# Kernel optimization log

Hardware: AMD Instinct MI355X
Metric: run time of the kernel (lower is better)

Reference implementation:

```python
import jax, jax.numpy as jnp
import numpy as np

B, S, HID, NH = 2, 2048, 1024, 16
HD = HID // NH
SCALE = HD ** -0.5


def elu_plus_one(x):
    return jax.nn.elu(x) + 1.0


def setup_inputs() -> dict:
    key = jax.random.key(0)
    ks = jax.random.split(key, 8)
    w_scale = 0.02  # keep logits in a sane range
    return {
        "hidden_states": jax.random.normal(ks[0], (B, S, HID), jnp.float32),
        "wq": jax.random.normal(ks[1], (HID, HID), jnp.float32) * w_scale,
        "wk": jax.random.normal(ks[2], (HID, HID), jnp.float32) * w_scale,
        "wv": jax.random.normal(ks[3], (HID, HID), jnp.float32) * w_scale,
        "wo": jax.random.normal(ks[4], (HID, HID), jnp.float32) * w_scale,
        "beta": jax.random.normal(ks[5], (NH,), jnp.float32),
        "memory": jax.random.normal(ks[6], (NH, HD, HD), jnp.float32),
        "memory_norm": jax.random.uniform(ks[7], (NH, HD), jnp.float32),
    }


def reference(hidden_states, wq, wk, wv, wo, beta, memory, memory_norm):
    b, s, _ = hidden_states.shape
    # nn.Linear(bias=False): x @ W^T; weights stored [out, in]
    def proj(x, w):
        return jnp.einsum("bsh,oh->bso", x, w).reshape(b, s, NH, HD).transpose(0, 2, 1, 3)

    q = proj(hidden_states, wq)  # [B,H,S,D]
    k = proj(hidden_states, wk)
    v = proj(hidden_states, wv)

    # local causal softmax attention (materializes [B,H,S,S] as the original does)
    scores = jnp.einsum("bhsd,bhtd->bhst", q, k) * SCALE
    causal_mask = jnp.triu(jnp.full((s, s), -jnp.inf, dtype=scores.dtype), k=1)
    attn = jax.nn.softmax(scores + causal_mask, axis=-1)
    a_local = jnp.einsum("bhst,bhtd->bhsd", attn, v)

    # compressive memory retrieval: sigma(Q) @ M / (sigma(Q) @ z)
    sigma_q = elu_plus_one(q)
    a_mem_unnorm = jnp.einsum("bhsd,hde->bhse", sigma_q, memory)
    norm = jnp.clip(jnp.einsum("bhsd,hd->bhs", sigma_q, memory_norm), 1e-6, None)
    a_mem = a_mem_unnorm / norm[..., None]

    gate = jax.nn.sigmoid(beta).reshape(1, NH, 1, 1)
    combined = gate * a_mem + (1.0 - gate) * a_local  # [B,H,S,D]
    combined = combined.transpose(0, 2, 1, 3).reshape(b, s, HID)
    return jnp.einsum("bsh,oh->bso", combined, wo)
```

## Files before the change

kernel.cpp:

```cpp
#include <hip/hip_runtime.h>
#include <stdint.h>

#define LOG2E 1.4426950408889634f

typedef __attribute__((ext_vector_type(8))) __bf16 bf16x8;
typedef __attribute__((ext_vector_type(4))) __bf16 bf16x4;
typedef __attribute__((ext_vector_type(4))) float f32x4;

__device__ inline void gll16(const void* g, void* l) {
  __builtin_amdgcn_global_load_lds(
      (const __attribute__((address_space(1))) void*)g,
      (__attribute__((address_space(3))) void*)l, 16, 0, 0);
}

__global__ __launch_bounds__(256) void cvt_all(
    const float* __restrict__ hs, const float* __restrict__ wq,
    const float* __restrict__ wk, const float* __restrict__ wv,
    const float* __restrict__ wo,
    __bf16* __restrict__ hsb, __bf16* __restrict__ wqb, __bf16* __restrict__ wkb,
    __bf16* __restrict__ wvb, __bf16* __restrict__ wob) {
  int bid = blockIdx.x;
  const float* s; __bf16* d; int i;
  if (bid < 4096) { s = hs; d = hsb; i = bid * 256 + threadIdx.x; }
  else {
    int seg = (bid - 4096) >> 10;
    i = ((bid - 4096) & 1023) * 256 + threadIdx.x;
    s = seg == 0 ? wq : seg == 1 ? wk : seg == 2 ? wv : wo;
    d = seg == 0 ? wqb : seg == 1 ? wkb : seg == 2 ? wvb : wob;
  }
  float4 v = ((const float4*)s)[i];
  bf16x4 o;
  o[0] = (__bf16)v.x; o[1] = (__bf16)v.y; o[2] = (__bf16)v.z; o[3] = (__bf16)v.w;
  *(bf16x4*)&d[(size_t)i * 4] = o;
}

#define KSCALE 0.18033688011112042f
#define QSWZ(row, col) (((row) << 6) + ((col) ^ (((row) & 7) << 3)))

__global__ __launch_bounds__(256, 3) void qkv_gemm(
    const __bf16* __restrict__ hsb, const __bf16* __restrict__ wqb,
    const __bf16* __restrict__ wkb, const __bf16* __restrict__ wvb,
    __bf16* __restrict__ qbuf, __bf16* __restrict__ kbuf,
    __bf16* __restrict__ vtb) {
  constexpr int K = 1024;
  __shared__ __align__(16) __bf16 lta[128 * 64];
  __shared__ __align__(16) __bf16 ltb[128 * 64];
  const int bid = blockIdx.x;
  const int z = bid >> 8, r = bid & 255;
  const __bf16 *A, *Bt;
  int m0, n0;
  if (z < 2) {
    A = hsb; Bt = z ? wkb : wqb;
    m0 = (r & 31) * 128; n0 = (r >> 5) * 128;
  } else {
    A = wvb; Bt = hsb;
    m0 = (r & 7) * 128; n0 = (r >> 3) * 128;
  }
  const int tid = threadIdx.x;
  const int w = tid >> 6, l = tid & 63;
  const int lg = l >> 4, lr = l & 15;
  const int wm = (w >> 1) * 64, wn = (w & 1) * 64;
  f32x4 acc[4][4] = {};
  const int srow = tid >> 3;
  const int scol = ((tid & 7) ^ ((tid >> 3) & 7)) * 8;
  const __bf16* ga = A + (size_t)(m0 + srow) * K + scol;
  const __bf16* gb = Bt + (size_t)(n0 + srow) * K + scol;
  for (int k0 = 0; k0 < K; k0 += 64) {
    __syncthreads();
#pragma unroll
    for (int p = 0; p < 4; ++p) {
      gll16(ga + (size_t)p * 32 * K + k0, &lta[p * 2048 + w * 512]);
      gll16(gb + (size_t)p * 32 * K + k0, &ltb[p * 2048 + w * 512]);
    }
    __syncthreads();
#pragma unroll
    for (int kk = 0; kk < 2; ++kk) {
      bf16x8 af[4], bfr[4];
#pragma unroll
      for (int i = 0; i < 4; ++i) {
        af[i]  = *(const bf16x8*)&lta[QSWZ(wm + i * 16 + lr, kk * 32 + lg * 8)];
        bfr[i] = *(const bf16x8*)&ltb[QSWZ(wn + i * 16 + lr, kk * 32 + lg * 8)];
      }
#pragma unroll
      for (int i = 0; i < 4; ++i)
#pragma unroll
        for (int j = 0; j < 4; ++j)
          acc[i][j] = __builtin_amdgcn_mfma_f32_16x16x32_bf16(af[i], bfr[j], acc[i][j], 0, 0, 0);
    }
  }
#pragma unroll
  for (int i = 0; i < 4; ++i)
#pragma unroll
    for (int j = 0; j < 4; ++j)
#pragma unroll
      for (int rr = 0; rr < 4; ++rr) {
        int gm = m0 + wm + i * 16 + lg * 4 + rr;
        int gn = n0 + wn + j * 16 + lr;
        float v = acc[i][j][rr];
        if (z < 2) {
          int bb = gm >> 11, s = gm & 2047, hh = gn >> 6, d = gn & 63;
          __bf16* dst = z ? kbuf : qbuf;
          if (z) v *= KSCALE;
          dst[(((size_t)bb * 16 + hh) * 2048 + s) * 64 + d] = (__bf16)v;
        } else {
          int bb = gn >> 11, s = gn & 2047, hh = gm >> 6, d = gm & 63;
          vtb[(((size_t)bb * 16 + hh) * 64 + d) * 2048 + s] = (__bf16)v;
        }
      }
}

__global__ __launch_bounds__(256, 4) void gemm_out(const __bf16* __restrict__ A,
                                                   const __bf16* __restrict__ Bt,
                                                   float* __restrict__ C,
                                                   int M, int N) {
  constexpr int K = 1024;
  __shared__ __align__(16) __bf16 lta[128 * 64];
  __shared__ __align__(16) __bf16 ltb[64 * 64];
  const int tid = threadIdx.x;
  const int w = tid >> 6, l = tid & 63;
  const int lg = l >> 4, lr = l & 15;
  const int m0 = blockIdx.x * 128, n0 = blockIdx.y * 64;
  const int wm = (w >> 1) * 64, wn = (w & 1) * 32;
  f32x4 acc[4][2] = {};
  const int srow = tid >> 3;
  const int scol = ((tid & 7) ^ ((tid >> 3) & 7)) * 8;
  const __bf16* ga = A + (size_t)(m0 + srow) * K + scol;
  const __bf16* gb = Bt + (size_t)(n0 + srow) * K + scol;
  for (int k0 = 0; k0 < K; k0 += 64) {
    __syncthreads();
#pragma unroll
    for (int p = 0; p < 4; ++p)
      gll16(ga + (size_t)p * 32 * K + k0, &lta[p * 2048 + w * 512]);
#pragma unroll
    for (int p = 0; p < 2; ++p)
      gll16(gb + (size_t)p * 32 * K + k0, &ltb[p * 2048 + w * 512]);
    __syncthreads();
#pragma unroll
    for (int kk = 0; kk < 2; ++kk) {
      bf16x8 af[4], bfr[2];
#pragma unroll
      for (int i = 0; i < 4; ++i)
        af[i]  = *(const bf16x8*)&lta[QSWZ(wm + i * 16 + lr, kk * 32 + lg * 8)];
#pragma unroll
      for (int j = 0; j < 2; ++j)
        bfr[j] = *(const bf16x8*)&ltb[QSWZ(wn + j * 16 + lr, kk * 32 + lg * 8)];
#pragma unroll
      for (int i = 0; i < 4; ++i)
#pragma unroll
        for (int j = 0; j < 2; ++j)
          acc[i][j] = __builtin_amdgcn_mfma_f32_16x16x32_bf16(af[i], bfr[j], acc[i][j], 0, 0, 0);
    }
  }
#pragma unroll
  for (int i = 0; i < 4; ++i)
#pragma unroll
    for (int j = 0; j < 2; ++j)
#pragma unroll
      for (int rr = 0; rr < 4; ++rr) {
        int gm = m0 + wm + i * 16 + lg * 4 + rr;
        int gn = n0 + wn + j * 16 + lr;
        C[(size_t)gm * N + gn] = acc[i][j][rr];
      }
}

#define DEFER_THR 11.5f
#define SWZ(row, col) (((row) << 7) + ((col) ^ (((row) & 7) << 3)))
#define SWZK(row, col) (((row) << 6) + ((col) ^ (((row) & 7) << 3)))

__global__ __launch_bounds__(256, 5) void attn_kernel(
    const __bf16* __restrict__ qb,
    const __bf16* __restrict__ kb,
    const __bf16* __restrict__ vtb,
    const float* __restrict__ memory,
    const float* __restrict__ memnorm,
    const float* __restrict__ beta,
    __bf16* __restrict__ comb)
{
  __shared__ __align__(16) __bf16 kt[128 * 64];
  __shared__ __align__(16) __bf16 vt[64 * 128];

  const int tid = threadIdx.x;
  const int w = tid >> 6, l = tid & 63;
  const int lg = l >> 4, lr = l & 15;
  const int t = 31 - (blockIdx.x >> 5);
  const int bh = blockIdx.x & 31;
  const int hh = bh & 15, b = bh >> 4;
  const int wq0 = t * 64 + w * 16;
  const int ntiles = (t >> 1) + 1;

  const int k_row = tid >> 3;
  const int k_col = ((tid & 7) ^ (k_row & 7)) * 8;
  const __bf16* ksrc = kb + ((size_t)bh * 2048 + k_row) * 64 + k_col;
  const int v_d = tid >> 4;
  const int v_col = ((tid & 15) ^ (v_d & 7)) * 8;
  const __bf16* vsrc = vtb + ((size_t)bh * 64 + v_d) * 2048 + v_col;
  __bf16* kdst = &kt[w * 512];
  __bf16* vdst = &vt[w * 512];

  bf16x8 qf[2];
#pragma unroll
  for (int kk = 0; kk < 2; ++kk)
    qf[kk] = *(const bf16x8*)(qb + ((size_t)bh * 2048 + wq0 + lr) * 64 + kk * 32 + lg * 8);

  float mrun = -1e30f, lsum = 0.f;
  f32x4 apv[4] = {};

  for (int kv = 0; kv < ntiles; ++kv) {
    const int kv0 = kv * 128;
    __syncthreads();
#pragma unroll
    for (int i = 0; i < 4; ++i)
      gll16(ksrc + (size_t)(kv0 + i * 32) * 64, kdst + i * 2048);
#pragma unroll
    for (int i = 0; i < 4; ++i)
      gll16(vsrc + (size_t)i * 16 * 2048 + kv0, vdst + i * 2048);
    asm volatile("s_waitcnt vmcnt(4)" ::: "memory");
    __builtin_amdgcn_sched_barrier(0);
    __builtin_amdgcn_s_barrier();

    f32x4 sc[8] = {};
    __builtin_amdgcn_s_setprio(1);
#pragma unroll
    for (int kk = 0; kk < 2; ++kk)
#pragma unroll
      for (int nf = 0; nf < 8; ++nf) {
        bf16x8 kf = *(const bf16x8*)&kt[SWZK(nf * 16 + lr, kk * 32 + lg * 8)];
        sc[nf] = __builtin_amdgcn_mfma_f32_16x16x32_bf16(kf, qf[kk], sc[nf], 0, 0, 0);
      }
    __builtin_amdgcn_s_setprio(0);

    const int qrow = wq0 + lr;
    if (kv == ntiles - 1) {
#pragma unroll
      for (int nf = 0; nf < 8; ++nf)
#pragma unroll
        for (int r = 0; r < 4; ++r)
          if (kv0 + nf * 16 + lg * 4 + r > qrow) sc[nf][r] = -1e30f;
    }

    f32x4 m4 = sc[0];
#pragma unroll
    for (int nf = 1; nf < 8; ++nf)
#pragma unroll
      for (int r = 0; r < 4; ++r) m4[r] = fmaxf(m4[r], sc[nf][r]);
    float mx = fmaxf(fmaxf(m4[0], m4[1]), fmaxf(m4[2], m4[3]));
    mx = fmaxf(mx, __shfl_xor(mx, 16, 64));
    mx = fmaxf(mx, __shfl_xor(mx, 32, 64));

    if (!__all(mx - mrun <= DEFER_THR)) {
      float mold = mrun;
      float mn = fmaxf(mold, mx);
      mrun = mn;
      float scl = __builtin_amdgcn_exp2f(mold - mn);
      lsum *= scl;
      float sclq[4];
#pragma unroll
      for (int r = 0; r < 4; ++r) sclq[r] = __shfl(scl, (lg << 2) | r, 16);
#pragma unroll
      for (int nf = 0; nf < 4; ++nf)
#pragma unroll
        for (int r = 0; r < 4; ++r) apv[nf][r] *= sclq[r];
    }

    f32x4 rs4 = {0.f, 0.f, 0.f, 0.f};
#pragma unroll
    for (int nf = 0; nf < 8; ++nf)
#pragma unroll
      for (int r = 0; r < 4; ++r) {
        float pv = __builtin_amdgcn_exp2f(sc[nf][r] - mrun);
        sc[nf][r] = pv;
        rs4[r] += pv;
      }
    float rs = (rs4[0] + rs4[1]) + (rs4[2] + rs4[3]);
    rs += __shfl_xor(rs, 16, 64);
    rs += __shfl_xor(rs, 32, 64);
    lsum += rs;

    asm volatile("s_waitcnt vmcnt(0)" ::: "memory");
    __builtin_amdgcn_sched_barrier(0);
    __builtin_amdgcn_s_barrier();

    __builtin_amdgcn_s_setprio(1);
#pragma unroll
    for (int kk = 0; kk < 4; ++kk) {
      uint32_t a0, a1, b0, b1;
      asm("v_cvt_pk_bf16_f32 %0, %1, %2" : "=v"(a0) : "v"(sc[2 * kk][0]), "v"(sc[2 * kk][1]));
      asm("v_cvt_pk_bf16_f32 %0, %1, %2" : "=v"(a1) : "v"(sc[2 * kk][2]), "v"(sc[2 * kk][3]));
      asm("v_cvt_pk_bf16_f32 %0, %1, %2" : "=v"(b0) : "v"(sc[2 * kk + 1][0]), "v"(sc[2 * kk + 1][1]));
      asm("v_cvt_pk_bf16_f32 %0, %1, %2" : "=v"(b1) : "v"(sc[2 * kk + 1][2]), "v"(sc[2 * kk + 1][3]));
      asm("v_permlane32_swap_b32 %0, %1" : "+v"(a0), "+v"(b0));
      asm("v_permlane32_swap_b32 %0, %1" : "+v"(a1), "+v"(b1));
      asm("v_permlane16_swap_b32 %0, %1" : "+v"(a0), "+v"(b0));
      asm("v_permlane16_swap_b32 %0, %1" : "+v"(a1), "+v"(b1));
      union { uint32_t u[4]; bf16x8 v; } pa;
      pa.u[0] = a0; pa.u[1] = a1; pa.u[2] = b0; pa.u[3] = b1;
#pragma unroll
      for (int nf = 0; nf < 4; ++nf) {
        bf16x8 vf = *(const bf16x8*)&vt[SWZ(nf * 16 + lr, kk * 32 + lg * 8)];
        apv[nf] = __builtin_amdgcn_mfma_f32_16x16x32_bf16(pa.v, vf, apv[nf], 0, 0, 0);
      }
    }
    __builtin_amdgcn_s_setprio(0);
  }

  __syncthreads();
  __bf16* mt = kt;
  for (int i = tid; i < 64 * 64; i += 256) {
    int d = i >> 6, e = i & 63;
    mt[e * 72 + d] = (__bf16)memory[((size_t)hh * 64 + d) * 64 + e];
  }
  for (int i = tid; i < 16 * 64; i += 256) {
    int e = 64 + (i >> 6), d = i & 63;
    mt[e * 72 + d] = (__bf16)memnorm[hh * 64 + d];
  }
  __syncthreads();

  bf16x8 sf[2];
#pragma unroll
  for (int kk = 0; kk < 2; ++kk) {
    bf16x8 q = qf[kk], s;
#pragma unroll
    for (int j = 0; j < 8; ++j) {
      float x = (float)q[j];
      float sg = x > 0.f ? x + 1.f : __builtin_amdgcn_exp2f(x * LOG2E);
      s[j] = (__bf16)sg;
    }
    sf[kk] = s;
  }

  f32x4 am[5] = {};
#pragma unroll
  for (int kk = 0; kk < 2; ++kk)
#pragma unroll
    for (int nf = 0; nf < 5; ++nf) {
      bf16x8 bb = *(const bf16x8*)&mt[(nf * 16 + lr) * 72 + kk * 32 + lg * 8];
      am[nf] = __builtin_amdgcn_mfma_f32_16x16x32_bf16(sf[kk], bb, am[nf], 0, 0, 0);
    }

  const float gate = 1.f / (1.f + __builtin_amdgcn_exp2f(-beta[hh] * LOG2E));
  const float og = 1.f - gate;
  float lsq[4];
#pragma unroll
  for (int r = 0; r < 4; ++r) lsq[r] = __shfl(lsum, (lg << 2) | r, 16);
#pragma unroll
  for (int r = 0; r < 4; ++r) {
    int row = wq0 + lg * 4 + r;
    float linv = __builtin_amdgcn_rcpf(lsq[r]);
    float nrm = fmaxf(am[4][r], 1e-6f);
    float ninv = __builtin_amdgcn_rcpf(nrm);
    size_t base = ((size_t)b * 2048 + row) * 1024 + hh * 64;
#pragma unroll
    for (int nf = 0; nf < 4; ++nf) {
      float al = apv[nf][r] * linv;
      float amv = am[nf][r] * ninv;
      comb[base + nf * 16 + lr] = (__bf16)(gate * amv + og * al);
    }
  }
}

extern "C" void kernel_launch(void* const* d_in, const int* in_sizes, int n_in,
                              void* d_out, int out_size, void* d_ws, size_t ws_size,
                              hipStream_t stream) {
  const float* hs      = (const float*)d_in[0];
  const float* wq      = (const float*)d_in[1];
  const float* wk      = (const float*)d_in[2];
  const float* wv      = (const float*)d_in[3];
  const float* wo      = (const float*)d_in[4];
  const float* beta    = (const float*)d_in[5];
  const float* memory  = (const float*)d_in[6];
  const float* memnorm = (const float*)d_in[7];
  float* out = (float*)d_out;

  char* ws = (char*)d_ws;
  __bf16* hsb  = (__bf16*)(ws);
  __bf16* wqb  = (__bf16*)(ws + ((size_t)8  << 20));
  __bf16* wkb  = (__bf16*)(ws + ((size_t)10 << 20));
  __bf16* wvb  = (__bf16*)(ws + ((size_t)12 << 20));
  __bf16* wob  = (__bf16*)(ws + ((size_t)14 << 20));
  __bf16* qbuf = (__bf16*)(ws + ((size_t)16 << 20));
  __bf16* kbuf = (__bf16*)(ws + ((size_t)24 << 20));
  __bf16* vtb  = (__bf16*)(ws + ((size_t)32 << 20));
  __bf16* comb = (__bf16*)(ws + ((size_t)40 << 20));

  cvt_all<<<8192, 256, 0, stream>>>(hs, wq, wk, wv, wo, hsb, wqb, wkb, wvb, wob);

  qkv_gemm<<<768, 256, 0, stream>>>(hsb, wqb, wkb, wvb, qbuf, kbuf, vtb);

  attn_kernel<<<1024, 256, 0, stream>>>(qbuf, kbuf, vtb, memory, memnorm, beta, comb);

  gemm_out<<<dim3(32, 16), 256, 0, stream>>>(comb, wob, out, 4096, 1024);
}
```

Baseline: 97.30 us.

## Double per-wave query rows in attention to reuse K/V tiles across two M-fragments

Each attention block now handles 128 query rows, with each wave owning 32 rows as two 16-row MFMA fragments. K and V tiles loaded into LDS are reused for twice as many rows, which halves the global loads and barriers per unit of work. The grid shrinks from 1024 to 512 blocks, the tile order is remapped to interleave heavy and light causal tiles, and launch bounds are relaxed to 2 blocks per CU. In exchange register pressure rises, occupancy drops and there are fewer blocks to balance across CUs.

```diff
diff --git a/kernel.cpp b/kernel.cpp
--- a/kernel.cpp
+++ b/kernel.cpp
@@ -167,7 +167,7 @@
 #define SWZ(row, col) (((row) << 7) + ((col) ^ (((row) & 7) << 3)))
 #define SWZK(row, col) (((row) << 6) + ((col) ^ (((row) & 7) << 3)))
 
-__global__ __launch_bounds__(256, 5) void attn_kernel(
+__global__ __launch_bounds__(256, 2) void attn_kernel(
     const __bf16* __restrict__ qb,
     const __bf16* __restrict__ kb,
     const __bf16* __restrict__ vtb,
@@ -182,11 +182,12 @@
   const int tid = threadIdx.x;
   const int w = tid >> 6, l = tid & 63;
   const int lg = l >> 4, lr = l & 15;
-  const int t = 31 - (blockIdx.x >> 5);
-  const int bh = blockIdx.x & 31;
+  const int bx = blockIdx.x;
+  const int t = (bx < 256) ? (15 - (bx >> 5)) : ((bx - 256) >> 5);
+  const int bh = bx & 31;
   const int hh = bh & 15, b = bh >> 4;
-  const int wq0 = t * 64 + w * 16;
-  const int ntiles = (t >> 1) + 1;
+  const int wq0 = t * 128 + w * 32;
+  const int ntiles = t + 1;
 
   const int k_row = tid >> 3;
   const int k_col = ((tid & 7) ^ (k_row & 7)) * 8;
@@ -197,13 +198,15 @@
   __bf16* kdst = &kt[w * 512];
   __bf16* vdst = &vt[w * 512];
 
-  bf16x8 qf[2];
-#pragma unroll
-  for (int kk = 0; kk < 2; ++kk)
-    qf[kk] = *(const bf16x8*)(qb + ((size_t)bh * 2048 + wq0 + lr) * 64 + kk * 32 + lg * 8);
-
-  float mrun = -1e30f, lsum = 0.f;
-  f32x4 apv[4] = {};
+  bf16x8 qf[2][2];
+#pragma unroll
+  for (int mf = 0; mf < 2; ++mf)
+#pragma unroll
+    for (int kk = 0; kk < 2; ++kk)
+      qf[mf][kk] = *(const bf16x8*)(qb + ((size_t)bh * 2048 + wq0 + mf * 16 + lr) * 64 + kk * 32 + lg * 8);
+
+  float mrun[2] = {-1e30f, -1e30f}, lsum[2] = {0.f, 0.f};
+  f32x4 apv[2][4] = {};
 
   for (int kv = 0; kv < ntiles; ++kv) {
     const int kv0 = kv * 128;
@@ -218,63 +221,70 @@
     __builtin_amdgcn_sched_barrier(0);
     __builtin_amdgcn_s_barrier();
 
-    f32x4 sc[8] = {};
+    f32x4 sc[2][8] = {};
     __builtin_amdgcn_s_setprio(1);
 #pragma unroll
     for (int kk = 0; kk < 2; ++kk)
 #pragma unroll
       for (int nf = 0; nf < 8; ++nf) {
         bf16x8 kf = *(const bf16x8*)&kt[SWZK(nf * 16 + lr, kk * 32 + lg * 8)];
-        sc[nf] = __builtin_amdgcn_mfma_f32_16x16x32_bf16(kf, qf[kk], sc[nf], 0, 0, 0);
+        sc[0][nf] = __builtin_amdgcn_mfma_f32_16x16x32_bf16(kf, qf[0][kk], sc[0][nf], 0, 0, 0);
+        sc[1][nf] = __builtin_amdgcn_mfma_f32_16x16x32_bf16(kf, qf[1][kk], sc[1][nf], 0, 0, 0);
       }
     __builtin_amdgcn_s_setprio(0);
 
-    const int qrow = wq0 + lr;
     if (kv == ntiles - 1) {
 #pragma unroll
+      for (int mf = 0; mf < 2; ++mf) {
+        const int qrow = wq0 + mf * 16 + lr;
+#pragma unroll
+        for (int nf = 0; nf < 8; ++nf)
+#pragma unroll
+          for (int r = 0; r < 4; ++r)
+            if (kv0 + nf * 16 + lg * 4 + r > qrow) sc[mf][nf][r] = -1e30f;
+      }
+    }
+
+#pragma unroll
+    for (int mf = 0; mf < 2; ++mf) {
+      f32x4 m4 = sc[mf][0];
+#pragma unroll
+      for (int nf = 1; nf < 8; ++nf)
+#pragma unroll
+        for (int r = 0; r < 4; ++r) m4[r] = fmaxf(m4[r], sc[mf][nf][r]);
+      float mx = fmaxf(fmaxf(m4[0], m4[1]), fmaxf(m4[2], m4[3]));
+      mx = fmaxf(mx, __shfl_xor(mx, 16, 64));
+      mx = fmaxf(mx, __shfl_xor(mx, 32, 64));
+
+      if (!__all(mx - mrun[mf] <= DEFER_THR)) {
+        float mold = mrun[mf];
+        float mn = fmaxf(mold, mx);
+        mrun[mf] = mn;
+        float scl = __builtin_amdgcn_exp2f(mold - mn);
+        lsum[mf] *= scl;
+        float sclq[4];
+#pragma unroll
+        for (int r = 0; r < 4; ++r) sclq[r] = __shfl(scl, (lg << 2) | r, 16);
+#pragma unroll
+        for (int nf = 0; nf < 4; ++nf)
+#pragma unroll
+          for (int r = 0; r < 4; ++r) apv[mf][nf][r] *= sclq[r];
+      }
+
+      f32x4 rs4 = {0.f, 0.f, 0.f, 0.f};
+#pragma unroll
       for (int nf = 0; nf < 8; ++nf)
 #pragma unroll
-        for (int r = 0; r < 4; ++r)
-          if (kv0 + nf * 16 + lg * 4 + r > qrow) sc[nf][r] = -1e30f;
-    }
-
-    f32x4 m4 = sc[0];
-#pragma unroll
-    for (int nf = 1; nf < 8; ++nf)
-#pragma unroll
-      for (int r = 0; r < 4; ++r) m4[r] = fmaxf(m4[r], sc[nf][r]);
-    float mx = fmaxf(fmaxf(m4[0], m4[1]), fmaxf(m4[2], m4[3]));
-    mx = fmaxf(mx, __shfl_xor(mx, 16, 64));
-    mx = fmaxf(mx, __shfl_xor(mx, 32, 64));
-
-    if (!__all(mx - mrun <= DEFER_THR)) {
-      float mold = mrun;
-      float mn = fmaxf(mold, mx);
-      mrun = mn;
-      float scl = __builtin_amdgcn_exp2f(mold - mn);
-      lsum *= scl;
-      float sclq[4];
-#pragma unroll
-      for (int r = 0; r < 4; ++r) sclq[r] = __shfl(scl, (lg << 2) | r, 16);
-#pragma unroll
-      for (int nf = 0; nf < 4; ++nf)
-#pragma unroll
-        for (int r = 0; r < 4; ++r) apv[nf][r] *= sclq[r];
-    }
-
-    f32x4 rs4 = {0.f, 0.f, 0.f, 0.f};
-#pragma unroll
-    for (int nf = 0; nf < 8; ++nf)
-#pragma unroll
-      for (int r = 0; r < 4; ++r) {
-        float pv = __builtin_amdgcn_exp2f(sc[nf][r] - mrun);
-        sc[nf][r] = pv;
-        rs4[r] += pv;
-      }
-    float rs = (rs4[0] + rs4[1]) + (rs4[2] + rs4[3]);
-    rs += __shfl_xor(rs, 16, 64);
-    rs += __shfl_xor(rs, 32, 64);
-    lsum += rs;
+        for (int r = 0; r < 4; ++r) {
+          float pv = __builtin_amdgcn_exp2f(sc[mf][nf][r] - mrun[mf]);
+          sc[mf][nf][r] = pv;
+          rs4[r] += pv;
+        }
+      float rs = (rs4[0] + rs4[1]) + (rs4[2] + rs4[3]);
+      rs += __shfl_xor(rs, 16, 64);
+      rs += __shfl_xor(rs, 32, 64);
+      lsum[mf] += rs;
+    }
 
     asm volatile("s_waitcnt vmcnt(0)" ::: "memory");
     __builtin_amdgcn_sched_barrier(0);
@@ -283,21 +293,25 @@
     __builtin_amdgcn_s_setprio(1);
 #pragma unroll
     for (int kk = 0; kk < 4; ++kk) {
-      uint32_t a0, a1, b0, b1;
-      asm("v_cvt_pk_bf16_f32 %0, %1, %2" : "=v"(a0) : "v"(sc[2 * kk][0]), "v"(sc[2 * kk][1]));
-      asm("v_cvt_pk_bf16_f32 %0, %1, %2" : "=v"(a1) : "v"(sc[2 * kk][2]), "v"(sc[2 * kk][3]));
-      asm("v_cvt_pk_bf16_f32 %0, %1, %2" : "=v"(b0) : "v"(sc[2 * kk + 1][0]), "v"(sc[2 * kk + 1][1]));
-      asm("v_cvt_pk_bf16_f32 %0, %1, %2" : "=v"(b1) : "v"(sc[2 * kk + 1][2]), "v"(sc[2 * kk + 1][3]));
-      asm("v_permlane32_swap_b32 %0, %1" : "+v"(a0), "+v"(b0));
-      asm("v_permlane32_swap_b32 %0, %1" : "+v"(a1), "+v"(b1));
-      asm("v_permlane16_swap_b32 %0, %1" : "+v"(a0), "+v"(b0));
-      asm("v_permlane16_swap_b32 %0, %1" : "+v"(a1), "+v"(b1));
-      union { uint32_t u[4]; bf16x8 v; } pa;
-      pa.u[0] = a0; pa.u[1] = a1; pa.u[2] = b0; pa.u[3] = b1;
+      union { uint32_t u[4]; bf16x8 v; } pa[2];
+#pragma unroll
+      for (int mf = 0; mf < 2; ++mf) {
+        uint32_t a0, a1, b0, b1;
+        asm("v_cvt_pk_bf16_f32 %0, %1, %2" : "=v"(a0) : "v"(sc[mf][2 * kk][0]), "v"(sc[mf][2 * kk][1]));
+        asm("v_cvt_pk_bf16_f32 %0, %1, %2" : "=v"(a1) : "v"(sc[mf][2 * kk][2]), "v"(sc[mf][2 * kk][3]));
+        asm("v_cvt_pk_bf16_f32 %0, %1, %2" : "=v"(b0) : "v"(sc[mf][2 * kk + 1][0]), "v"(sc[mf][2 * kk + 1][1]));
+        asm("v_cvt_pk_bf16_f32 %0, %1, %2" : "=v"(b1) : "v"(sc[mf][2 * kk + 1][2]), "v"(sc[mf][2 * kk + 1][3]));
+        asm("v_permlane32_swap_b32 %0, %1" : "+v"(a0), "+v"(b0));
+        asm("v_permlane32_swap_b32 %0, %1" : "+v"(a1), "+v"(b1));
+        asm("v_permlane16_swap_b32 %0, %1" : "+v"(a0), "+v"(b0));
+        asm("v_permlane16_swap_b32 %0, %1" : "+v"(a1), "+v"(b1));
+        pa[mf].u[0] = a0; pa[mf].u[1] = a1; pa[mf].u[2] = b0; pa[mf].u[3] = b1;
+      }
 #pragma unroll
       for (int nf = 0; nf < 4; ++nf) {
         bf16x8 vf = *(const bf16x8*)&vt[SWZ(nf * 16 + lr, kk * 32 + lg * 8)];
-        apv[nf] = __builtin_amdgcn_mfma_f32_16x16x32_bf16(pa.v, vf, apv[nf], 0, 0, 0);
+        apv[0][nf] = __builtin_amdgcn_mfma_f32_16x16x32_bf16(pa[0].v, vf, apv[0][nf], 0, 0, 0);
+        apv[1][nf] = __builtin_amdgcn_mfma_f32_16x16x32_bf16(pa[1].v, vf, apv[1][nf], 0, 0, 0);
       }
     }
     __builtin_amdgcn_s_setprio(0);
@@ -315,45 +329,51 @@
   }
   __syncthreads();
 
-  bf16x8 sf[2];
-#pragma unroll
-  for (int kk = 0; kk < 2; ++kk) {
-    bf16x8 q = qf[kk], s;
-#pragma unroll
-    for (int j = 0; j < 8; ++j) {
-      float x = (float)q[j];
-      float sg = x > 0.f ? x + 1.f : __builtin_amdgcn_exp2f(x * LOG2E);
-      s[j] = (__bf16)sg;
-    }
-    sf[kk] = s;
-  }
-
-  f32x4 am[5] = {};
+  bf16x8 sf[2][2];
+#pragma unroll
+  for (int mf = 0; mf < 2; ++mf)
+#pragma unroll
+    for (int kk = 0; kk < 2; ++kk) {
+      bf16x8 q = qf[mf][kk], s;
+#pragma unroll
+      for (int j = 0; j < 8; ++j) {
+        float x = (float)q[j];
+        float sg = x > 0.f ? x + 1.f : __builtin_amdgcn_exp2f(x * LOG2E);
+        s[j] = (__bf16)sg;
+      }
+      sf[mf][kk] = s;
+    }
+
+  f32x4 am[2][5] = {};
 #pragma unroll
   for (int kk = 0; kk < 2; ++kk)
 #pragma unroll
     for (int nf = 0; nf < 5; ++nf) {
       bf16x8 bb = *(const bf16x8*)&mt[(nf * 16 + lr) * 72 + kk * 32 + lg * 8];
-      am[nf] = __builtin_amdgcn_mfma_f32_16x16x32_bf16(sf[kk], bb, am[nf], 0, 0, 0);
+      am[0][nf] = __builtin_amdgcn_mfma_f32_16x16x32_bf16(sf[0][kk], bb, am[0][nf], 0, 0, 0);
+      am[1][nf] = __builtin_amdgcn_mfma_f32_16x16x32_bf16(sf[1][kk], bb, am[1][nf], 0, 0, 0);
     }
 
   const float gate = 1.f / (1.f + __builtin_amdgcn_exp2f(-beta[hh] * LOG2E));
   const float og = 1.f - gate;
-  float lsq[4];
-#pragma unroll
-  for (int r = 0; r < 4; ++r) lsq[r] = __shfl(lsum, (lg << 2) | r, 16);
-#pragma unroll
-  for (int r = 0; r < 4; ++r) {
-    int row = wq0 + lg * 4 + r;
-    float linv = __builtin_amdgcn_rcpf(lsq[r]);
-    float nrm = fmaxf(am[4][r], 1e-6f);
-    float ninv = __builtin_amdgcn_rcpf(nrm);
-    size_t base = ((size_t)b * 2048 + row) * 1024 + hh * 64;
-#pragma unroll
-    for (int nf = 0; nf < 4; ++nf) {
-      float al = apv[nf][r] * linv;
-      float amv = am[nf][r] * ninv;
-      comb[base + nf * 16 + lr] = (__bf16)(gate * amv + og * al);
+#pragma unroll
+  for (int mf = 0; mf < 2; ++mf) {
+    float lsq[4];
+#pragma unroll
+    for (int r = 0; r < 4; ++r) lsq[r] = __shfl(lsum[mf], (lg << 2) | r, 16);
+#pragma unroll
+    for (int r = 0; r < 4; ++r) {
+      int row = wq0 + mf * 16 + lg * 4 + r;
+      float linv = __builtin_amdgcn_rcpf(lsq[r]);
+      float nrm = fmaxf(am[mf][4][r], 1e-6f);
+      float ninv = __builtin_amdgcn_rcpf(nrm);
+      size_t base = ((size_t)b * 2048 + row) * 1024 + hh * 64;
+#pragma unroll
+      for (int nf = 0; nf < 4; ++nf) {
+        float al = apv[mf][nf][r] * linv;
+        float amv = am[mf][nf][r] * ninv;
+        comb[base + nf * 16 + lr] = (__bf16)(gate * amv + og * al);
+      }
     }
   }
 }
@@ -386,7 +406,7 @@
 
   qkv_gemm<<<768, 256, 0, stream>>>(hsb, wqb, wkb, wvb, qbuf, kbuf, vtb);
 
-  attn_kernel<<<1024, 256, 0, stream>>>(qbuf, kbuf, vtb, memory, memnorm, beta, comb);
+  attn_kernel<<<512, 256, 0, stream>>>(qbuf, kbuf, vtb, memory, memnorm, beta, comb);
 
   gemm_out<<<dim3(32, 16), 256, 0, stream>>>(comb, wob, out, 4096, 1024);
 }
```

Measured after the change: 102.2 us. 5.0% more time.

## Merge Q and K projection tiles into 512-thread blocks sharing the A tile

Applied to the files above, without the earlier changes.

The QKV GEMM now runs 384 blocks of 512 threads instead of 768 blocks of 256. For Q/K, each block computes both the Q and the K tile for the same hidden-state rows, so the A tile is loaded into LDS once and shared by two 4-wave halves. For V, each block covers a 128x256 tile. The aim is to cut redundant global loads and LDS fills of the activation tile. In exchange, LDS use per block rises to 48KB, occupancy drops, and the number of blocks is halved, which can hurt wave scheduling.

```diff
diff --git a/kernel.cpp b/kernel.cpp
--- a/kernel.cpp
+++ b/kernel.cpp
@@ -37,40 +37,63 @@
 #define KSCALE 0.18033688011112042f
 #define QSWZ(row, col) (((row) << 6) + ((col) ^ (((row) & 7) << 3)))
 
-__global__ __launch_bounds__(256, 3) void qkv_gemm(
+__global__ __launch_bounds__(512, 2) void qkv_gemm(
     const __bf16* __restrict__ hsb, const __bf16* __restrict__ wqb,
     const __bf16* __restrict__ wkb, const __bf16* __restrict__ wvb,
     __bf16* __restrict__ qbuf, __bf16* __restrict__ kbuf,
     __bf16* __restrict__ vtb) {
   constexpr int K = 1024;
-  __shared__ __align__(16) __bf16 lta[128 * 64];
-  __shared__ __align__(16) __bf16 ltb[128 * 64];
+  __shared__ __align__(16) __bf16 lds[3 * 8192];
+  __bf16* lta = lds;
+  __bf16* ltb1 = lds + 8192;
+  __bf16* ltb2 = lds + 16384;
+
   const int bid = blockIdx.x;
-  const int z = bid >> 8, r = bid & 255;
-  const __bf16 *A, *Bt;
-  int m0, n0;
-  if (z < 2) {
-    A = hsb; Bt = z ? wkb : wqb;
-    m0 = (r & 31) * 128; n0 = (r >> 5) * 128;
-  } else {
-    A = wvb; Bt = hsb;
-    m0 = (r & 7) * 128; n0 = (r >> 3) * 128;
-  }
+  const bool isqk = bid < 256;
   const int tid = threadIdx.x;
   const int w = tid >> 6, l = tid & 63;
   const int lg = l >> 4, lr = l & 15;
-  const int wm = (w >> 1) * 64, wn = (w & 1) * 64;
+  const int ltid = tid & 255;
+  const int hi = w >> 2;
+  const int ws = w & 3;
+
+  int m0, n0;
+  const __bf16 *Abase, *B1base, *B2base;
+  if (isqk) {
+    m0 = (bid & 31) * 128; n0 = (bid >> 5) * 128;
+    Abase = hsb; B1base = wqb; B2base = wkb;
+  } else {
+    int r = bid - 256;
+    m0 = (r & 7) * 128; n0 = (r >> 3) * 256;
+    Abase = wvb; B1base = hsb; B2base = hsb;
+  }
+
+  const int srow = ltid >> 3;
+  const int scol = ((ltid & 7) ^ ((ltid >> 3) & 7)) * 8;
+  const __bf16* ga  = Abase + (size_t)(m0 + srow) * K + scol;
+  const __bf16* gb1 = B1base + (size_t)(n0 + srow) * K + scol;
+  const __bf16* gb2 = isqk ? (B2base + (size_t)(n0 + srow) * K + scol)
+                           : (B1base + (size_t)(n0 + 128 + srow) * K + scol);
+  const int wq4 = (w & 3) * 512;
+
+  int wm, wn;
+  __bf16* ltb;
+  if (isqk) { wm = (ws >> 1) * 64; wn = (ws & 1) * 64; ltb = hi ? ltb2 : ltb1; }
+  else      { wm = hi * 64;        wn = ws * 64;       ltb = ltb1; }
+
   f32x4 acc[4][4] = {};
-  const int srow = tid >> 3;
-  const int scol = ((tid & 7) ^ ((tid >> 3) & 7)) * 8;
-  const __bf16* ga = A + (size_t)(m0 + srow) * K + scol;
-  const __bf16* gb = Bt + (size_t)(n0 + srow) * K + scol;
   for (int k0 = 0; k0 < K; k0 += 64) {
     __syncthreads();
-#pragma unroll
-    for (int p = 0; p < 4; ++p) {
-      gll16(ga + (size_t)p * 32 * K + k0, &lta[p * 2048 + w * 512]);
-      gll16(gb + (size_t)p * 32 * K + k0, &ltb[p * 2048 + w * 512]);
+    if (w < 4) {
+#pragma unroll
+      for (int p = 0; p < 4; ++p) {
+        gll16(ga  + (size_t)p * 32 * K + k0, &lta[p * 2048 + wq4]);
+        gll16(gb1 + (size_t)p * 32 * K + k0, &ltb1[p * 2048 + wq4]);
+      }
+    } else {
+#pragma unroll
+      for (int p = 0; p < 4; ++p)
+        gll16(gb2 + (size_t)p * 32 * K + k0, &ltb2[p * 2048 + wq4]);
     }
     __syncthreads();
 #pragma unroll
@@ -88,6 +111,7 @@
           acc[i][j] = __builtin_amdgcn_mfma_f32_16x16x32_bf16(af[i], bfr[j], acc[i][j], 0, 0, 0);
     }
   }
+
 #pragma unroll
   for (int i = 0; i < 4; ++i)
 #pragma unroll
@@ -97,11 +121,13 @@
         int gm = m0 + wm + i * 16 + lg * 4 + rr;
         int gn = n0 + wn + j * 16 + lr;
         float v = acc[i][j][rr];
-        if (z < 2) {
+        if (isqk) {
           int bb = gm >> 11, s = gm & 2047, hh = gn >> 6, d = gn & 63;
-          __bf16* dst = z ? kbuf : qbuf;
-          if (z) v *= KSCALE;
-          dst[(((size_t)bb * 16 + hh) * 2048 + s) * 64 + d] = (__bf16)v;
+          if (hi) {
+            kbuf[(((size_t)bb * 16 + hh) * 2048 + s) * 64 + d] = (__bf16)(v * KSCALE);
+          } else {
+            qbuf[(((size_t)bb * 16 + hh) * 2048 + s) * 64 + d] = (__bf16)v;
+          }
         } else {
           int bb = gn >> 11, s = gn & 2047, hh = gm >> 6, d = gm & 63;
           vtb[(((size_t)bb * 16 + hh) * 64 + d) * 2048 + s] = (__bf16)v;
@@ -384,7 +410,7 @@
 
   cvt_all<<<8192, 256, 0, stream>>>(hs, wq, wk, wv, wo, hsb, wqb, wkb, wvb, wob);
 
-  qkv_gemm<<<768, 256, 0, stream>>>(hsb, wqb, wkb, wvb, qbuf, kbuf, vtb);
+  qkv_gemm<<<384, 512, 0, stream>>>(hsb, wqb, wkb, wvb, qbuf, kbuf, vtb);
 
   attn_kernel<<<1024, 256, 0, stream>>>(qbuf, kbuf, vtb, memory, memnorm, beta, comb);
 
```

Result: slower. 99.30 us (+2.1%).
